# Kernel optimization log

Measured on AMD Instinct MI355X. Metric: run time of the kernel, lower is better.

Reference implementation:

```python
import jax, jax.numpy as jnp
import numpy as np

D = 1024
F = 256
EPS = 1e-5


def layer_norm(x, g, b):
    mu = jnp.mean(x, axis=-1, keepdims=True)
    var = jnp.mean((x - mu) ** 2, axis=-1, keepdims=True)
    return (x - mu) * jax.lax.rsqrt(var + EPS) * g + b


def setup_inputs() -> dict:
    key = jax.random.key(0)
    ks = jax.random.split(key, 8)
    B, S = 4, 4096
    return {
        "bottom_up_input": jax.random.normal(ks[0], (B, S, D), dtype=jnp.float32),
        "top_down_prediction": jax.random.normal(ks[1], (B, S, D), dtype=jnp.float32),
        "W_spec": jax.random.normal(ks[2], (2 * F, D), dtype=jnp.float32) * 0.02,
        "log_decay": jnp.linspace(-3.0, -0.001, F, dtype=jnp.float32),
        "frequencies": jax.random.normal(ks[3], (F,), dtype=jnp.float32) * 0.1,
        "W_from": jax.random.normal(ks[4], (D, 2 * F), dtype=jnp.float32) * 0.02,
        "ln1_g": jnp.ones((D,), jnp.float32),
        "ln1_b": jnp.zeros((D,), jnp.float32),
        "W1": jax.random.normal(ks[5], (D, D), dtype=jnp.float32) * 0.02,
        "b1": jnp.zeros((D,), jnp.float32),
        "W2": jax.random.normal(ks[6], (D, D), dtype=jnp.float32) * 0.02,
        "b2": jnp.zeros((D,), jnp.float32),
        "ln2_g": jnp.ones((D,), jnp.float32),
        "ln2_b": jnp.zeros((D,), jnp.float32),
        "error_weight": jnp.asarray(0.1, jnp.float32),
    }


def spectral_conv(x, W_spec, log_decay, frequencies, W_from, ln1_g, ln1_b):
    # x: [B,S,D]
    x = layer_norm(x, ln1_g, ln1_b)
    B, S, _ = x.shape
    spectral = jnp.einsum('bsd,fd->bsf', x, W_spec)  # [B,S,2F]
    u = jax.lax.complex(spectral[..., :F], spectral[..., F:])  # [B,S,F] complex
    decay = jax.nn.sigmoid(log_decay)
    omega = jnp.tanh(frequencies) * 0.1  # dt = 1.0
    rot = jax.lax.complex(jnp.cos(omega), jnp.sin(omega))  # [F]
    A = (decay * rot).astype(jnp.complex64)  # [F]
    # kernel[t] = A^t * rot, built with cumprod as in the original
    ones = jnp.ones((1, F), dtype=A.dtype)
    A_seq = jnp.broadcast_to(A[None, :], (S - 1, F))
    powers = jnp.cumprod(jnp.concatenate([ones, A_seq], axis=0), axis=0)  # [S,F]
    kernel = (powers * rot[None, :])[None]  # [1,S,F]
    n_fft = 2 * S
    U_f = jnp.fft.fft(u, n=n_fft, axis=1)
    K_f = jnp.fft.fft(kernel, n=n_fft, axis=1)
    y = jnp.fft.ifft(U_f * K_f, n=n_fft, axis=1)[:, :S, :]  # [B,S,F]
    spectral_out = jnp.concatenate([y.real, y.imag], axis=-1)  # [B,S,2F]
    return jnp.einsum('bsf,df->bsd', spectral_out, W_from)


def reference(bottom_up_input, top_down_prediction, W_spec, log_decay, frequencies,
              W_from, ln1_g, ln1_b, W1, b1, W2, b2, ln2_g, ln2_b, error_weight):
    bu_repr = spectral_conv(bottom_up_input, W_spec, log_decay, frequencies,
                            W_from, ln1_g, ln1_b)
    error = jnp.clip(bu_repr - top_down_prediction, -1.0, 1.0)
    corrected = bu_repr - jax.nn.sigmoid(error_weight) * error
    prediction_error = jnp.clip(jnp.mean(error ** 2), 0.0, 1.0)
    h = jax.nn.gelu(jnp.einsum('bsd,ed->bse', corrected, W1) + b1, approximate=False)
    h = jnp.einsum('bsd,ed->bse', h, W2) + b2
    next_prediction = layer_norm(h, ln2_g, ln2_b)
    return corrected, next_prediction, prediction_error
```

## Files before the change

kernel.cpp:

```cpp
#include <hip/hip_runtime.h>
#include <math.h>

#define Dn 1024
#define Fn 256
#define Sn 4096
#define Bn 4
#define Mn (Bn*Sn)
#define CHn 64
#define NCn (Sn/CHn)

typedef __bf16 bf16x8 __attribute__((ext_vector_type(8)));
typedef float  f32x4  __attribute__((ext_vector_type(4)));

__device__ inline unsigned short f2bf(float f) {
  unsigned int u = __float_as_uint(f);
  u += 0x7fffu + ((u >> 16) & 1u);
  return (unsigned short)(u >> 16);
}
__device__ inline float bf2f(unsigned short s) {
  return __uint_as_float(((unsigned int)s) << 16);
}

__device__ inline void async16(const void* g, void* l) {
  __builtin_amdgcn_global_load_lds(
      (__attribute__((address_space(1))) void*)(g),
      (__attribute__((address_space(3))) void*)(l), 16, 0, 0);
}

#define WAITVM(n) __builtin_amdgcn_s_waitcnt(0xF70 | (n))
#define BARRIER() asm volatile("s_barrier" ::: "memory")

__global__ __launch_bounds__(256) void convert_weights(
    const float* __restrict__ wspec, const float* __restrict__ wfrom,
    const float* __restrict__ w1, const float* __restrict__ w2,
    unsigned short* __restrict__ o_spec, unsigned short* __restrict__ o_from,
    unsigned short* __restrict__ o_w1, unsigned short* __restrict__ o_w2) {
  int i = blockIdx.x * 256 + threadIdx.x;
  if (i < 524288) {
    o_spec[i] = f2bf(wspec[i]);
    o_from[i] = f2bf(wfrom[i]);
  }
  o_w1[i] = f2bf(w1[i]);
  o_w2[i] = f2bf(w2[i]);
}

template <int IN_BF16, int OUT_BF16>
__global__ __launch_bounds__(256) void ln_kernel(
    const void* __restrict__ xin, const float* __restrict__ g,
    const float* __restrict__ b, void* __restrict__ out) {
  int row = blockIdx.x, tid = threadIdx.x;
  int wid = tid >> 6, lane = tid & 63;
  float4 v;
  if (IN_BF16) {
    ushort4 u = ((const ushort4*)xin)[(size_t)row * 256 + tid];
    v.x = bf2f(u.x); v.y = bf2f(u.y); v.z = bf2f(u.z); v.w = bf2f(u.w);
  } else {
    v = ((const float4*)xin)[(size_t)row * 256 + tid];
  }
  float s  = v.x + v.y + v.z + v.w;
  float ss = v.x * v.x + v.y * v.y + v.z * v.z + v.w * v.w;
  #pragma unroll
  for (int o = 32; o; o >>= 1) {
    s  += __shfl_down(s, o);
    ss += __shfl_down(ss, o);
  }
  __shared__ float r1[4], r2[4];
  if (lane == 0) { r1[wid] = s; r2[wid] = ss; }
  __syncthreads();
  s  = r1[0] + r1[1] + r1[2] + r1[3];
  ss = r2[0] + r2[1] + r2[2] + r2[3];
  float mu  = s * (1.0f / Dn);
  float var = ss * (1.0f / Dn) - mu * mu;
  float rs  = rsqrtf(var + 1e-5f);
  float4 gv = ((const float4*)g)[tid];
  float4 bv = ((const float4*)b)[tid];
  float o0 = (v.x - mu) * rs * gv.x + bv.x;
  float o1 = (v.y - mu) * rs * gv.y + bv.y;
  float o2 = (v.z - mu) * rs * gv.z + bv.z;
  float o3 = (v.w - mu) * rs * gv.w + bv.w;
  if (OUT_BF16) {
    ushort4 w;
    w.x = f2bf(o0); w.y = f2bf(o1); w.z = f2bf(o2); w.w = f2bf(o3);
    ((ushort4*)out)[(size_t)row * 256 + tid] = w;
  } else {
    float4 w; w.x = o0; w.y = o1; w.z = o2; w.w = o3;
    ((float4*)out)[(size_t)row * 256 + tid] = w;
  }
}

template <int MODE>
__global__ __launch_bounds__(256, 4) void gemm_bt(
    const unsigned short* __restrict__ A, const unsigned short* __restrict__ Bw,
    int K, int N,
    float* __restrict__ outF, unsigned short* __restrict__ outH,
    const float* __restrict__ td, const float* __restrict__ bias,
    const float* __restrict__ ew, float* __restrict__ errAcc) {
  __shared__ unsigned short As[2 * 4096];
  __shared__ unsigned short Bs[2 * 4096];
  __shared__ float red[4];

  int tid = threadIdx.x;
  int wid = tid >> 6, lane = tid & 63;
  int wm = wid >> 1, wn = wid & 1;
  int quad = lane >> 4, l16 = lane & 15;

  int g = blockIdx.x + gridDim.x * blockIdx.y;
  int nbn = gridDim.x;
  int gh = g >> 3;
  int bn = gh % nbn;
  int bm = (g & 7) + (gh / nbn) * 8;

  int r_lo = lane >> 2;
  int c8   = (lane & 3) * 8;

  const unsigned short* Abase = A + (size_t)bm * 128 * K;
  const unsigned short* Bbase = Bw + (size_t)bn * 128 * K;

  f32x4 acc[4][4] = {};

  const int T = K >> 5;
  auto issue = [&](int t, int stg) {
    int k0 = t << 5;
    #pragma unroll
    for (int s = 0; s < 2; ++s) {
      int chunk = s * 4 + wid;
      int r = chunk * 16 + r_lo;
      async16(Abase + (size_t)r * K + k0 + c8, As + stg * 4096 + chunk * 512);
      async16(Bbase + (size_t)r * K + k0 + c8, Bs + stg * 4096 + chunk * 512);
    }
  };

  issue(0, 0);

  for (int k = 0; k < T; ++k) {
    WAITVM(0);
    BARRIER();
    if (k + 1 < T) issue(k + 1, (k + 1) & 1);

    const unsigned short* Ab = As + (k & 1) * 4096;
    const unsigned short* Bb = Bs + (k & 1) * 4096;
    bf16x8 af[4], bf[4];
    #pragma unroll
    for (int i = 0; i < 4; i++)
      af[i] = *(const bf16x8*)(Ab + (wm * 64 + i * 16 + l16) * 32 + quad * 8);
    #pragma unroll
    for (int j = 0; j < 4; j++)
      bf[j] = *(const bf16x8*)(Bb + (wn * 64 + j * 16 + l16) * 32 + quad * 8);
    #pragma unroll
    for (int i = 0; i < 4; i++)
      #pragma unroll
      for (int j = 0; j < 4; j++)
        acc[i][j] = __builtin_amdgcn_mfma_f32_16x16x32_bf16(af[i], bf[j], acc[i][j], 0, 0, 0);
  }

  float esum = 0.0f;
  float sigw = 0.0f;
  if (MODE == 1) sigw = 1.0f / (1.0f + expf(-ew[0]));

  #pragma unroll
  for (int i = 0; i < 4; i++) {
    int row_base = bm * 128 + wm * 64 + i * 16 + quad * 4;
    #pragma unroll
    for (int j = 0; j < 4; j++) {
      int col = bn * 128 + wn * 64 + j * 16 + l16;
      #pragma unroll
      for (int r = 0; r < 4; r++) {
        size_t idx = (size_t)(row_base + r) * N + col;
        float v = acc[i][j][r];
        if (MODE == 0) {
          outH[idx] = f2bf(v);
        } else if (MODE == 1) {
          float e = v - td[idx];
          e = fminf(fmaxf(e, -1.0f), 1.0f);
          float corr = v - sigw * e;
          outF[idx] = corr;
          outH[idx] = f2bf(corr);
          esum += e * e;
        } else if (MODE == 2) {
          float h = v + bias[col];
          float gel = 0.5f * h * (1.0f + erff(h * 0.70710678118654752f));
          outH[idx] = f2bf(gel);
        } else if (MODE == 3) {
          outF[idx] = v + bias[col];
        } else {
          outH[idx] = f2bf(v + bias[col]);
        }
      }
    }
  }

  if (MODE == 1) {
    #pragma unroll
    for (int o = 32; o; o >>= 1) esum += __shfl_down(esum, o);
    if (lane == 0) red[wid] = esum;
    __syncthreads();
    if (tid == 0) atomicAdd(errAcc, red[0] + red[1] + red[2] + red[3]);
  }
}

template <int MODE, int NBN>
__global__ __launch_bounds__(512, 2) void gemm256(
    const unsigned short* __restrict__ A, const unsigned short* __restrict__ Bw,
    int K,
    float* __restrict__ outF, unsigned short* __restrict__ outH,
    const float* __restrict__ td, const float* __restrict__ bias,
    const float* __restrict__ ew, float* __restrict__ errAcc) {
  __shared__ unsigned short As[2 * 16384];
  __shared__ unsigned short Bs[2 * 16384];
  __shared__ float red[8];

  const int tid = threadIdx.x;
  const int w = tid >> 6, l = tid & 63;
  const int wm = w >> 2, wn = w & 3;
  const int quad = l >> 4, l16 = l & 15;
  const int sw = l16 & 7;
  const int N = NBN * 256;

  int g = blockIdx.x;
  int gh = g >> 3;
  int bn = gh % NBN;
  int bm = (g & 7) + (gh / NBN) * 8;

  const int r8 = w * 8 + (l >> 3);
  const int gcol = ((l & 7) ^ (l >> 3)) * 8;
  const unsigned short* Ag = A + (size_t)(bm * 256 + r8) * K + gcol;
  const unsigned short* Bg = Bw + (size_t)(bn * 256 + r8) * K + gcol;

  auto stage = [&](int t, int c) {
    const int k0 = t << 6;
    #pragma unroll
    for (int i = 0; i < 4; i++) {
      async16(Ag + (size_t)(i * 64) * K + k0, As + c * 16384 + i * 4096 + w * 512);
      async16(Bg + (size_t)(i * 64) * K + k0, Bs + c * 16384 + i * 4096 + w * 512);
    }
  };

  f32x4 acc[8][4] = {};
  const int NT = K >> 6;

  stage(0, 0);
  stage(1, 1);
  WAITVM(8);
  BARRIER();

  for (int t = 0; t < NT; ++t) {
    const int c = t & 1;
    const unsigned short* Ab = As + c * 16384;
    const unsigned short* Bb = Bs + c * 16384;
    bf16x8 af[8], bfr[4];

    #pragma unroll
    for (int m = 0; m < 8; m++)
      af[m] = *(const bf16x8*)(Ab + (wm * 128 + m * 16 + l16) * 64 + ((quad ^ sw) << 3));
    #pragma unroll
    for (int n = 0; n < 4; n++)
      bfr[n] = *(const bf16x8*)(Bb + (wn * 64 + n * 16 + l16) * 64 + ((quad ^ sw) << 3));
    BARRIER();
    __builtin_amdgcn_s_setprio(1);
    #pragma unroll
    for (int m = 0; m < 8; m++) {
      acc[m][0] = __builtin_amdgcn_mfma_f32_16x16x32_bf16(af[m], bfr[0], acc[m][0], 0, 0, 0);
      acc[m][1] = __builtin_amdgcn_mfma_f32_16x16x32_bf16(af[m], bfr[1], acc[m][1], 0, 0, 0);
    }
    __builtin_amdgcn_s_setprio(0);
    BARRIER();

    __builtin_amdgcn_s_setprio(1);
    #pragma unroll
    for (int m = 0; m < 8; m++) {
      acc[m][2] = __builtin_amdgcn_mfma_f32_16x16x32_bf16(af[m], bfr[2], acc[m][2], 0, 0, 0);
      acc[m][3] = __builtin_amdgcn_mfma_f32_16x16x32_bf16(af[m], bfr[3], acc[m][3], 0, 0, 0);
    }
    __builtin_amdgcn_s_setprio(0);
    BARRIER();

    #pragma unroll
    for (int m = 0; m < 8; m++)
      af[m] = *(const bf16x8*)(Ab + (wm * 128 + m * 16 + l16) * 64 + (((4 + quad) ^ sw) << 3));
    #pragma unroll
    for (int n = 0; n < 4; n++)
      bfr[n] = *(const bf16x8*)(Bb + (wn * 64 + n * 16 + l16) * 64 + (((4 + quad) ^ sw) << 3));
    BARRIER();
    __builtin_amdgcn_s_setprio(1);
    #pragma unroll
    for (int m = 0; m < 8; m++) {
      acc[m][0] = __builtin_amdgcn_mfma_f32_16x16x32_bf16(af[m], bfr[0], acc[m][0], 0, 0, 0);
      acc[m][1] = __builtin_amdgcn_mfma_f32_16x16x32_bf16(af[m], bfr[1], acc[m][1], 0, 0, 0);
    }
    __builtin_amdgcn_s_setprio(0);
    BARRIER();

    if (t + 2 < NT) { stage(t + 2, c); WAITVM(8); }
    else            { WAITVM(0); }
    BARRIER();
    __builtin_amdgcn_s_setprio(1);
    #pragma unroll
    for (int m = 0; m < 8; m++) {
      acc[m][2] = __builtin_amdgcn_mfma_f32_16x16x32_bf16(af[m], bfr[2], acc[m][2], 0, 0, 0);
      acc[m][3] = __builtin_amdgcn_mfma_f32_16x16x32_bf16(af[m], bfr[3], acc[m][3], 0, 0, 0);
    }
    __builtin_amdgcn_s_setprio(0);
    BARRIER();
  }

  float esum = 0.0f;
  float sigw = 0.0f;
  if (MODE == 1) sigw = 1.0f / (1.0f + expf(-ew[0]));

  #pragma unroll
  for (int m = 0; m < 8; m++) {
    int row_base = bm * 256 + wm * 128 + m * 16 + quad * 4;
    #pragma unroll
    for (int n = 0; n < 4; n++) {
      int col = bn * 256 + wn * 64 + n * 16 + l16;
      #pragma unroll
      for (int r = 0; r < 4; r++) {
        size_t idx = (size_t)(row_base + r) * N + col;
        float v = acc[m][n][r];
        if (MODE == 0) {
          outH[idx] = f2bf(v);
        } else if (MODE == 1) {
          float e = v - td[idx];
          e = fminf(fmaxf(e, -1.0f), 1.0f);
          float corr = v - sigw * e;
          outF[idx] = corr;
          outH[idx] = f2bf(corr);
          esum += e * e;
        } else if (MODE == 2) {
          float h = v + bias[col];
          float gel = 0.5f * h * (1.0f + erff(h * 0.70710678118654752f));
          outH[idx] = f2bf(gel);
        } else if (MODE == 3) {
          outF[idx] = v + bias[col];
        } else {
          outH[idx] = f2bf(v + bias[col]);
        }
      }
    }
  }

  if (MODE == 1) {
    #pragma unroll
    for (int o = 32; o; o >>= 1) esum += __shfl_down(esum, o);
    if (l == 0) red[w] = esum;
    __syncthreads();
    if (tid == 0) {
      float s = 0.0f;
      #pragma unroll
      for (int i = 0; i < 8; i++) s += red[i];
      atomicAdd(errAcc, s);
    }
  }
}

__global__ __launch_bounds__(256) void scan_partial(
    const unsigned short* __restrict__ spec, const float* __restrict__ log_decay,
    const float* __restrict__ freq, float2* __restrict__ chunkfin) {
  int f = threadIdx.x;
  int bx = blockIdx.x;
  int b = bx / NCn, c = bx % NCn;
  float dec = 1.0f / (1.0f + expf(-log_decay[f]));
  float om  = tanhf(freq[f]) * 0.1f;
  float Are = dec * cosf(om), Aim = dec * sinf(om);
  const unsigned short* u = spec + ((size_t)b * Sn + (size_t)c * CHn) * 512 + f;
  float sre = 0.0f, sim = 0.0f;
  for (int t = 0; t < CHn; t++) {
    float ure = bf2f(u[(size_t)t * 512]);
    float uim = bf2f(u[(size_t)t * 512 + 256]);
    float nre = Are * sre - Aim * sim + ure;
    float nim = Are * sim + Aim * sre + uim;
    sre = nre; sim = nim;
  }
  chunkfin[(size_t)bx * 256 + f] = make_float2(sre, sim);
}

__global__ __launch_bounds__(256) void scan_carry(
    const float* __restrict__ log_decay, const float* __restrict__ freq,
    const float2* __restrict__ chunkfin, float2* __restrict__ carries) {
  int f = threadIdx.x;
  int b = blockIdx.x;
  float dec = 1.0f / (1.0f + expf(-log_decay[f]));
  float om  = tanhf(freq[f]) * 0.1f;
  float pre = dec * cosf(om), pim = dec * sinf(om);
  #pragma unroll
  for (int i = 0; i < 6; i++) {
    float nr = pre * pre - pim * pim;
    float ni = 2.0f * pre * pim;
    pre = nr; pim = ni;
  }
  float sre = 0.0f, sim = 0.0f;
  for (int c = 0; c < NCn; c++) {
    carries[(size_t)(b * NCn + c) * 256 + f] = make_float2(sre, sim);
    float2 cf = chunkfin[(size_t)(b * NCn + c) * 256 + f];
    float nre = pre * sre - pim * sim + cf.x;
    float nim = pre * sim + pim * sre + cf.y;
    sre = nre; sim = nim;
  }
}

__global__ __launch_bounds__(256) void scan_final(
    const unsigned short* __restrict__ spec, const float* __restrict__ log_decay,
    const float* __restrict__ freq, const float2* __restrict__ carries,
    unsigned short* __restrict__ outH) {
  int f = threadIdx.x;
  int bx = blockIdx.x;
  int b = bx / NCn, c = bx % NCn;
  float dec = 1.0f / (1.0f + expf(-log_decay[f]));
  float om  = tanhf(freq[f]) * 0.1f;
  float Are = dec * cosf(om), Aim = dec * sinf(om);
  float Rre = cosf(om), Rim = sinf(om);
  float2 s0 = carries[(size_t)bx * 256 + f];
  float sre = s0.x, sim = s0.y;
  const unsigned short* u = spec + ((size_t)b * Sn + (size_t)c * CHn) * 512 + f;
  unsigned short* o = outH + ((size_t)b * Sn + (size_t)c * CHn) * 512 + f;
  for (int t = 0; t < CHn; t++) {
    float ure = bf2f(u[(size_t)t * 512]);
    float uim = bf2f(u[(size_t)t * 512 + 256]);
    float nre = Are * sre - Aim * sim + ure;
    float nim = Are * sim + Aim * sre + uim;
    sre = nre; sim = nim;
    o[(size_t)t * 512]       = f2bf(Rre * sre - Rim * sim);
    o[(size_t)t * 512 + 256] = f2bf(Rre * sim + Rim * sre);
  }
}

__global__ void finalize_err(const float* __restrict__ errAcc, float* __restrict__ out) {
  float m = errAcc[0] * (1.0f / 16777216.0f);
  out[0] = fminf(fmaxf(m, 0.0f), 1.0f);
}

extern "C" void kernel_launch(void* const* d_in, const int* in_sizes, int n_in,
                              void* d_out, int out_size, void* d_ws, size_t ws_size,
                              hipStream_t stream) {
  (void)in_sizes; (void)n_in; (void)out_size; (void)ws_size;
  const float* x     = (const float*)d_in[0];
  const float* td    = (const float*)d_in[1];
  const float* wspec = (const float*)d_in[2];
  const float* logd  = (const float*)d_in[3];
  const float* freq  = (const float*)d_in[4];
  const float* wfrom = (const float*)d_in[5];
  const float* g1    = (const float*)d_in[6];
  const float* b1ln  = (const float*)d_in[7];
  const float* W1    = (const float*)d_in[8];
  const float* b1    = (const float*)d_in[9];
  const float* W2    = (const float*)d_in[10];
  const float* b2    = (const float*)d_in[11];
  const float* g2    = (const float*)d_in[12];
  const float* b2ln  = (const float*)d_in[13];
  const float* ew    = (const float*)d_in[14];

  char* ws = (char*)d_ws;
  size_t off = 0;
  float* errAcc = (float*)(ws + off);              off += 256;
  unsigned short* wspec_h = (unsigned short*)(ws + off); off += (size_t)512 * 1024 * 2;
  unsigned short* wfrom_h = (unsigned short*)(ws + off); off += (size_t)1024 * 512 * 2;
  unsigned short* w1_h    = (unsigned short*)(ws + off); off += (size_t)1024 * 1024 * 2;
  unsigned short* w2_h    = (unsigned short*)(ws + off); off += (size_t)1024 * 1024 * 2;
  unsigned short* xn_h   = (unsigned short*)(ws + off);
  unsigned short* corr_h = (unsigned short*)(ws + off);
  unsigned short* h2_h   = (unsigned short*)(ws + off); off += (size_t)Mn * 1024 * 2;
  unsigned short* spec  = (unsigned short*)(ws + off);
  unsigned short* h1_h  = (unsigned short*)(ws + off);  off += (size_t)Mn * 1024 * 2;
  unsigned short* so_h = (unsigned short*)(ws + off);  off += (size_t)Mn * 512 * 2;
  float2* chunkfin = (float2*)(ws + off);              off += (size_t)Bn * NCn * 256 * 8;
  float2* carries  = (float2*)(ws + off);              off += (size_t)Bn * NCn * 256 * 8;

  float* outCorr = (float*)d_out;
  float* outNP   = outCorr + (size_t)Mn * 1024;
  float* outErr  = outNP + (size_t)Mn * 1024;

  hipMemsetAsync(errAcc, 0, 4, stream);
  convert_weights<<<4096, 256, 0, stream>>>(wspec, wfrom, W1, W2,
                                            wspec_h, wfrom_h, w1_h, w2_h);
  ln_kernel<0, 1><<<Mn, 256, 0, stream>>>(x, g1, b1ln, xn_h);
  gemm_bt<0><<<dim3(512 / 128, Mn / 128), 256, 0, stream>>>(
      xn_h, wspec_h, 1024, 512, nullptr, spec, nullptr, nullptr, nullptr, nullptr);
  scan_partial<<<Bn * NCn, 256, 0, stream>>>(spec, logd, freq, chunkfin);
  scan_carry<<<Bn, 256, 0, stream>>>(logd, freq, chunkfin, carries);
  scan_final<<<Bn * NCn, 256, 0, stream>>>(spec, logd, freq, carries, so_h);
  gemm256<1, 4><<<256, 512, 0, stream>>>(
      so_h, wfrom_h, 512, outCorr, corr_h, td, nullptr, ew, errAcc);
  gemm256<2, 4><<<256, 512, 0, stream>>>(
      corr_h, w1_h, 1024, nullptr, h1_h, nullptr, b1, nullptr, nullptr);
  gemm256<4, 4><<<256, 512, 0, stream>>>(
      h1_h, w2_h, 1024, nullptr, h2_h, nullptr, b2, nullptr, nullptr);
  ln_kernel<1, 0><<<Mn, 256, 0, stream>>>(h2_h, g2, b2ln, outNP);
  finalize_err<<<1, 1, 0, stream>>>(errAcc, outErr);
}
```

Baseline: 465.4 us.

## Fuse weight conversion into LN1, restructure chunked scan, merge finalize into LN2

Weight conversion to bf16 now shares a launch with the first layer norm, which uses one wavefront per row with shuffle-only reductions. The error finalize step moves into the second layer-norm kernel. The three-kernel chunked scan becomes two kernels with chunk size 16: each wave handles one chunk across four frequencies with vectorized loads, and the carry is recomputed per chunk by a serial loop over preceding chunk finals instead of a separate carry kernel. The W_from projection switches from gemm256<1> to gemm_bt<1>. The goal is fewer launches and a better-parallelized scan, but the per-chunk carry recomputation adds quadratic work in the chunk count.

```diff
diff --git a/kernel.cpp b/kernel.cpp
--- a/kernel.cpp
+++ b/kernel.cpp
@@ -6,7 +6,7 @@
 #define Sn 4096
 #define Bn 4
 #define Mn (Bn*Sn)
-#define CHn 64
+#define CHn 16
 #define NCn (Sn/CHn)
 
 typedef __bf16 bf16x8 __attribute__((ext_vector_type(8)));
@@ -30,61 +30,95 @@
 #define WAITVM(n) __builtin_amdgcn_s_waitcnt(0xF70 | (n))
 #define BARRIER() asm volatile("s_barrier" ::: "memory")
 
-__global__ __launch_bounds__(256) void convert_weights(
+__global__ __launch_bounds__(256) void ln1_conv(
+    const float* __restrict__ x, const float* __restrict__ g,
+    const float* __restrict__ b, unsigned short* __restrict__ out,
     const float* __restrict__ wspec, const float* __restrict__ wfrom,
     const float* __restrict__ w1, const float* __restrict__ w2,
     unsigned short* __restrict__ o_spec, unsigned short* __restrict__ o_from,
     unsigned short* __restrict__ o_w1, unsigned short* __restrict__ o_w2) {
-  int i = blockIdx.x * 256 + threadIdx.x;
-  if (i < 524288) {
-    o_spec[i] = f2bf(wspec[i]);
-    o_from[i] = f2bf(wfrom[i]);
-  }
-  o_w1[i] = f2bf(w1[i]);
-  o_w2[i] = f2bf(w2[i]);
-}
-
-template <int IN_BF16, int OUT_BF16>
-__global__ __launch_bounds__(256) void ln_kernel(
-    const void* __restrict__ xin, const float* __restrict__ g,
-    const float* __restrict__ b, void* __restrict__ out) {
-  int row = blockIdx.x, tid = threadIdx.x;
+  int tid = threadIdx.x;
+  int gid = blockIdx.x * 256 + tid;
+  o_w1[gid] = f2bf(w1[gid]);
+  o_w2[gid] = f2bf(w2[gid]);
+  if (gid < 524288) {
+    o_spec[gid] = f2bf(wspec[gid]);
+    o_from[gid] = f2bf(wfrom[gid]);
+  }
+
   int wid = tid >> 6, lane = tid & 63;
-  float4 v;
-  if (IN_BF16) {
-    ushort4 u = ((const ushort4*)xin)[(size_t)row * 256 + tid];
-    v.x = bf2f(u.x); v.y = bf2f(u.y); v.z = bf2f(u.z); v.w = bf2f(u.w);
-  } else {
-    v = ((const float4*)xin)[(size_t)row * 256 + tid];
-  }
-  float s  = v.x + v.y + v.z + v.w;
-  float ss = v.x * v.x + v.y * v.y + v.z * v.z + v.w * v.w;
+  int row = blockIdx.x * 4 + wid;
+  const float4* xr = (const float4*)x + (size_t)row * 256;
+  float4 v[4];
+  float s = 0.0f, ss = 0.0f;
+  #pragma unroll
+  for (int k = 0; k < 4; k++) {
+    v[k] = xr[lane + 64 * k];
+    s  += v[k].x + v[k].y + v[k].z + v[k].w;
+    ss += v[k].x * v[k].x + v[k].y * v[k].y + v[k].z * v[k].z + v[k].w * v[k].w;
+  }
   #pragma unroll
   for (int o = 32; o; o >>= 1) {
-    s  += __shfl_down(s, o);
-    ss += __shfl_down(ss, o);
-  }
-  __shared__ float r1[4], r2[4];
-  if (lane == 0) { r1[wid] = s; r2[wid] = ss; }
-  __syncthreads();
-  s  = r1[0] + r1[1] + r1[2] + r1[3];
-  ss = r2[0] + r2[1] + r2[2] + r2[3];
+    s  += __shfl_xor(s, o);
+    ss += __shfl_xor(ss, o);
+  }
   float mu  = s * (1.0f / Dn);
   float var = ss * (1.0f / Dn) - mu * mu;
   float rs  = rsqrtf(var + 1e-5f);
-  float4 gv = ((const float4*)g)[tid];
-  float4 bv = ((const float4*)b)[tid];
-  float o0 = (v.x - mu) * rs * gv.x + bv.x;
-  float o1 = (v.y - mu) * rs * gv.y + bv.y;
-  float o2 = (v.z - mu) * rs * gv.z + bv.z;
-  float o3 = (v.w - mu) * rs * gv.w + bv.w;
-  if (OUT_BF16) {
+  ushort4* orow = (ushort4*)out + (size_t)row * 256;
+  #pragma unroll
+  for (int k = 0; k < 4; k++) {
+    float4 gv = ((const float4*)g)[lane + 64 * k];
+    float4 bv = ((const float4*)b)[lane + 64 * k];
     ushort4 w;
-    w.x = f2bf(o0); w.y = f2bf(o1); w.z = f2bf(o2); w.w = f2bf(o3);
-    ((ushort4*)out)[(size_t)row * 256 + tid] = w;
-  } else {
-    float4 w; w.x = o0; w.y = o1; w.z = o2; w.w = o3;
-    ((float4*)out)[(size_t)row * 256 + tid] = w;
+    w.x = f2bf((v[k].x - mu) * rs * gv.x + bv.x);
+    w.y = f2bf((v[k].y - mu) * rs * gv.y + bv.y);
+    w.z = f2bf((v[k].z - mu) * rs * gv.z + bv.z);
+    w.w = f2bf((v[k].w - mu) * rs * gv.w + bv.w);
+    orow[lane + 64 * k] = w;
+  }
+}
+
+__global__ __launch_bounds__(256) void ln2_err(
+    const unsigned short* __restrict__ h, const float* __restrict__ g,
+    const float* __restrict__ b, float* __restrict__ out,
+    const float* __restrict__ errAcc, float* __restrict__ outErr) {
+  int tid = threadIdx.x;
+  if (blockIdx.x == 0 && tid == 0) {
+    float m = errAcc[0] * (1.0f / 16777216.0f);
+    outErr[0] = fminf(fmaxf(m, 0.0f), 1.0f);
+  }
+  int wid = tid >> 6, lane = tid & 63;
+  int row = blockIdx.x * 4 + wid;
+  const ushort4* xr = (const ushort4*)h + (size_t)row * 256;
+  float4 v[4];
+  float s = 0.0f, ss = 0.0f;
+  #pragma unroll
+  for (int k = 0; k < 4; k++) {
+    ushort4 u = xr[lane + 64 * k];
+    v[k].x = bf2f(u.x); v[k].y = bf2f(u.y); v[k].z = bf2f(u.z); v[k].w = bf2f(u.w);
+    s  += v[k].x + v[k].y + v[k].z + v[k].w;
+    ss += v[k].x * v[k].x + v[k].y * v[k].y + v[k].z * v[k].z + v[k].w * v[k].w;
+  }
+  #pragma unroll
+  for (int o = 32; o; o >>= 1) {
+    s  += __shfl_xor(s, o);
+    ss += __shfl_xor(ss, o);
+  }
+  float mu  = s * (1.0f / Dn);
+  float var = ss * (1.0f / Dn) - mu * mu;
+  float rs  = rsqrtf(var + 1e-5f);
+  float4* orow = (float4*)out + (size_t)row * 256;
+  #pragma unroll
+  for (int k = 0; k < 4; k++) {
+    float4 gv = ((const float4*)g)[lane + 64 * k];
+    float4 bv = ((const float4*)b)[lane + 64 * k];
+    float4 w;
+    w.x = (v[k].x - mu) * rs * gv.x + bv.x;
+    w.y = (v[k].y - mu) * rs * gv.y + bv.y;
+    w.z = (v[k].z - mu) * rs * gv.z + bv.z;
+    w.w = (v[k].w - mu) * rs * gv.w + bv.w;
+    orow[lane + 64 * k] = w;
   }
 }
 
@@ -356,77 +390,92 @@
 __global__ __launch_bounds__(256) void scan_partial(
     const unsigned short* __restrict__ spec, const float* __restrict__ log_decay,
     const float* __restrict__ freq, float2* __restrict__ chunkfin) {
-  int f = threadIdx.x;
-  int bx = blockIdx.x;
-  int b = bx / NCn, c = bx % NCn;
-  float dec = 1.0f / (1.0f + expf(-log_decay[f]));
-  float om  = tanhf(freq[f]) * 0.1f;
-  float Are = dec * cosf(om), Aim = dec * sinf(om);
-  const unsigned short* u = spec + ((size_t)b * Sn + (size_t)c * CHn) * 512 + f;
-  float sre = 0.0f, sim = 0.0f;
+  int tid = threadIdx.x, wid = tid >> 6, lane = tid & 63;
+  int chunk = blockIdx.x * 4 + wid;
+  int b = chunk >> 8, c = chunk & (NCn - 1);
+  int f0 = lane * 4;
+  float Are[4], Aim[4];
+  #pragma unroll
+  for (int k = 0; k < 4; k++) {
+    float dec = 1.0f / (1.0f + expf(-log_decay[f0 + k]));
+    float om  = tanhf(freq[f0 + k]) * 0.1f;
+    Are[k] = dec * cosf(om); Aim[k] = dec * sinf(om);
+  }
+  const unsigned short* u = spec + ((size_t)b * Sn + (size_t)c * CHn) * 512;
+  float sre[4] = {0, 0, 0, 0}, sim[4] = {0, 0, 0, 0};
   for (int t = 0; t < CHn; t++) {
-    float ure = bf2f(u[(size_t)t * 512]);
-    float uim = bf2f(u[(size_t)t * 512 + 256]);
-    float nre = Are * sre - Aim * sim + ure;
-    float nim = Are * sim + Aim * sre + uim;
-    sre = nre; sim = nim;
-  }
-  chunkfin[(size_t)bx * 256 + f] = make_float2(sre, sim);
-}
-
-__global__ __launch_bounds__(256) void scan_carry(
-    const float* __restrict__ log_decay, const float* __restrict__ freq,
-    const float2* __restrict__ chunkfin, float2* __restrict__ carries) {
-  int f = threadIdx.x;
-  int b = blockIdx.x;
-  float dec = 1.0f / (1.0f + expf(-log_decay[f]));
-  float om  = tanhf(freq[f]) * 0.1f;
-  float pre = dec * cosf(om), pim = dec * sinf(om);
-  #pragma unroll
-  for (int i = 0; i < 6; i++) {
-    float nr = pre * pre - pim * pim;
-    float ni = 2.0f * pre * pim;
-    pre = nr; pim = ni;
-  }
-  float sre = 0.0f, sim = 0.0f;
-  for (int c = 0; c < NCn; c++) {
-    carries[(size_t)(b * NCn + c) * 256 + f] = make_float2(sre, sim);
-    float2 cf = chunkfin[(size_t)(b * NCn + c) * 256 + f];
-    float nre = pre * sre - pim * sim + cf.x;
-    float nim = pre * sim + pim * sre + cf.y;
-    sre = nre; sim = nim;
-  }
-}
-
-__global__ __launch_bounds__(256) void scan_final(
+    ushort4 ur = *(const ushort4*)(u + (size_t)t * 512 + f0);
+    ushort4 ui = *(const ushort4*)(u + (size_t)t * 512 + 256 + f0);
+    float urf[4] = {bf2f(ur.x), bf2f(ur.y), bf2f(ur.z), bf2f(ur.w)};
+    float uif[4] = {bf2f(ui.x), bf2f(ui.y), bf2f(ui.z), bf2f(ui.w)};
+    #pragma unroll
+    for (int k = 0; k < 4; k++) {
+      float nre = Are[k] * sre[k] - Aim[k] * sim[k] + urf[k];
+      float nim = Are[k] * sim[k] + Aim[k] * sre[k] + uif[k];
+      sre[k] = nre; sim[k] = nim;
+    }
+  }
+  float2* cf = chunkfin + (size_t)chunk * 256 + f0;
+  #pragma unroll
+  for (int k = 0; k < 4; k++) cf[k] = make_float2(sre[k], sim[k]);
+}
+
+__global__ __launch_bounds__(256) void scan_cf(
     const unsigned short* __restrict__ spec, const float* __restrict__ log_decay,
-    const float* __restrict__ freq, const float2* __restrict__ carries,
+    const float* __restrict__ freq, const float2* __restrict__ chunkfin,
     unsigned short* __restrict__ outH) {
-  int f = threadIdx.x;
-  int bx = blockIdx.x;
-  int b = bx / NCn, c = bx % NCn;
-  float dec = 1.0f / (1.0f + expf(-log_decay[f]));
-  float om  = tanhf(freq[f]) * 0.1f;
-  float Are = dec * cosf(om), Aim = dec * sinf(om);
-  float Rre = cosf(om), Rim = sinf(om);
-  float2 s0 = carries[(size_t)bx * 256 + f];
-  float sre = s0.x, sim = s0.y;
-  const unsigned short* u = spec + ((size_t)b * Sn + (size_t)c * CHn) * 512 + f;
-  unsigned short* o = outH + ((size_t)b * Sn + (size_t)c * CHn) * 512 + f;
+  int tid = threadIdx.x, wid = tid >> 6, lane = tid & 63;
+  int chunk = blockIdx.x * 4 + wid;
+  int b = chunk >> 8, c = chunk & (NCn - 1);
+  int f0 = lane * 4;
+  float Are[4], Aim[4], Rre[4], Rim[4], Pre[4], Pim[4];
+  #pragma unroll
+  for (int k = 0; k < 4; k++) {
+    float dec = 1.0f / (1.0f + expf(-log_decay[f0 + k]));
+    float om  = tanhf(freq[f0 + k]) * 0.1f;
+    Rre[k] = cosf(om); Rim[k] = sinf(om);
+    Are[k] = dec * Rre[k]; Aim[k] = dec * Rim[k];
+    float pre = Are[k], pim = Aim[k];
+    #pragma unroll
+    for (int i = 0; i < 4; i++) {
+      float nr = pre * pre - pim * pim;
+      float ni = 2.0f * pre * pim;
+      pre = nr; pim = ni;
+    }
+    Pre[k] = pre; Pim[k] = pim;
+  }
+  float sre[4] = {0, 0, 0, 0}, sim[4] = {0, 0, 0, 0};
+  const float2* cfb = chunkfin + (size_t)b * NCn * 256;
+  for (int j = 0; j < c; j++) {
+    #pragma unroll
+    for (int k = 0; k < 4; k++) {
+      float2 cf = cfb[(size_t)j * 256 + f0 + k];
+      float nre = Pre[k] * sre[k] - Pim[k] * sim[k] + cf.x;
+      float nim = Pre[k] * sim[k] + Pim[k] * sre[k] + cf.y;
+      sre[k] = nre; sim[k] = nim;
+    }
+  }
+  const unsigned short* u = spec + ((size_t)b * Sn + (size_t)c * CHn) * 512;
+  unsigned short* o = outH + ((size_t)b * Sn + (size_t)c * CHn) * 512;
   for (int t = 0; t < CHn; t++) {
-    float ure = bf2f(u[(size_t)t * 512]);
-    float uim = bf2f(u[(size_t)t * 512 + 256]);
-    float nre = Are * sre - Aim * sim + ure;
-    float nim = Are * sim + Aim * sre + uim;
-    sre = nre; sim = nim;
-    o[(size_t)t * 512]       = f2bf(Rre * sre - Rim * sim);
-    o[(size_t)t * 512 + 256] = f2bf(Rre * sim + Rim * sre);
-  }
-}
-
-__global__ void finalize_err(const float* __restrict__ errAcc, float* __restrict__ out) {
-  float m = errAcc[0] * (1.0f / 16777216.0f);
-  out[0] = fminf(fmaxf(m, 0.0f), 1.0f);
+    ushort4 ur = *(const ushort4*)(u + (size_t)t * 512 + f0);
+    ushort4 ui = *(const ushort4*)(u + (size_t)t * 512 + 256 + f0);
+    float urf[4] = {bf2f(ur.x), bf2f(ur.y), bf2f(ur.z), bf2f(ur.w)};
+    float uif[4] = {bf2f(ui.x), bf2f(ui.y), bf2f(ui.z), bf2f(ui.w)};
+    ushort4 wr, wi;
+    unsigned short* wrp = &wr.x;
+    unsigned short* wip = &wi.x;
+    #pragma unroll
+    for (int k = 0; k < 4; k++) {
+      float nre = Are[k] * sre[k] - Aim[k] * sim[k] + urf[k];
+      float nim = Are[k] * sim[k] + Aim[k] * sre[k] + uif[k];
+      sre[k] = nre; sim[k] = nim;
+      wrp[k] = f2bf(Rre[k] * sre[k] - Rim[k] * sim[k]);
+      wip[k] = f2bf(Rre[k] * sim[k] + Rim[k] * sre[k]);
+    }
+    *(ushort4*)(o + (size_t)t * 512 + f0) = wr;
+    *(ushort4*)(o + (size_t)t * 512 + 256 + f0) = wi;
+  }
 }
 
 extern "C" void kernel_launch(void* const* d_in, const int* in_sizes, int n_in,
@@ -463,27 +512,24 @@
   unsigned short* h1_h  = (unsigned short*)(ws + off);  off += (size_t)Mn * 1024 * 2;
   unsigned short* so_h = (unsigned short*)(ws + off);  off += (size_t)Mn * 512 * 2;
   float2* chunkfin = (float2*)(ws + off);              off += (size_t)Bn * NCn * 256 * 8;
-  float2* carries  = (float2*)(ws + off);              off += (size_t)Bn * NCn * 256 * 8;
 
   float* outCorr = (float*)d_out;
   float* outNP   = outCorr + (size_t)Mn * 1024;
   float* outErr  = outNP + (size_t)Mn * 1024;
 
   hipMemsetAsync(errAcc, 0, 4, stream);
-  convert_weights<<<4096, 256, 0, stream>>>(wspec, wfrom, W1, W2,
-                                            wspec_h, wfrom_h, w1_h, w2_h);
-  ln_kernel<0, 1><<<Mn, 256, 0, stream>>>(x, g1, b1ln, xn_h);
+  ln1_conv<<<4096, 256, 0, stream>>>(x, g1, b1ln, xn_h,
+                                     wspec, wfrom, W1, W2,
+                                     wspec_h, wfrom_h, w1_h, w2_h);
   gemm_bt<0><<<dim3(512 / 128, Mn / 128), 256, 0, stream>>>(
       xn_h, wspec_h, 1024, 512, nullptr, spec, nullptr, nullptr, nullptr, nullptr);
-  scan_partial<<<Bn * NCn, 256, 0, stream>>>(spec, logd, freq, chunkfin);
-  scan_carry<<<Bn, 256, 0, stream>>>(logd, freq, chunkfin, carries);
-  scan_final<<<Bn * NCn, 256, 0, stream>>>(spec, logd, freq, carries, so_h);
-  gemm256<1, 4><<<256, 512, 0, stream>>>(
-      so_h, wfrom_h, 512, outCorr, corr_h, td, nullptr, ew, errAcc);
+  scan_partial<<<256, 256, 0, stream>>>(spec, logd, freq, chunkfin);
+  scan_cf<<<256, 256, 0, stream>>>(spec, logd, freq, chunkfin, so_h);
+  gemm_bt<1><<<dim3(1024 / 128, Mn / 128), 256, 0, stream>>>(
+      so_h, wfrom_h, 512, 1024, outCorr, corr_h, td, nullptr, ew, errAcc);
   gemm256<2, 4><<<256, 512, 0, stream>>>(
       corr_h, w1_h, 1024, nullptr, h1_h, nullptr, b1, nullptr, nullptr);
   gemm256<4, 4><<<256, 512, 0, stream>>>(
       h1_h, w2_h, 1024, nullptr, h2_h, nullptr, b2, nullptr, nullptr);
-  ln_kernel<1, 0><<<Mn, 256, 0, stream>>>(h2_h, g2, b2ln, outNP);
-  finalize_err<<<1, 1, 0, stream>>>(errAcc, outErr);
-}
+  ln2_err<<<4096, 256, 0, stream>>>(h2_h, g2, b2ln, outNP, errAcc, outErr);
+}
```

After: 533.6 us. 1.15x slower.
